# Performance work log

Measured on AMD Instinct MI355X. Metric: run time of the kernel, lower is better.

## Reference

```python
import jax, jax.numpy as jnp
import numpy as np

D = 2048          # hidden_size
E = 32            # num_experts
DFF = 1024        # moe_intermediate_size
T = 1024          # tokens (batch*seq)
TOP_K = 4         # num_experts_per_token
N_GROUP = 4
TOPK_GROUP = 2
SCALING = 2.5     # routed_scaling_factor
N_SHARED = 1
SHARED_DFF = DFF * N_SHARED


def setup_inputs() -> dict:
    key = jax.random.key(0)
    ks = jax.random.split(key, 9)
    def init(k, shape, fan_in):
        return jax.random.normal(k, shape, jnp.float32) * (fan_in ** -0.5)
    return {
        "x": jax.random.normal(ks[0], (T, D), jnp.float32),
        "gate_w": init(ks[1], (E, D), D),                 # router Linear weight [out,in]
        "bias": jnp.zeros((E,), jnp.float32),             # e_score_correction_bias
        "Wg": init(ks[2], (E, DFF, D), D),                # expert gate_proj
        "Wu": init(ks[3], (E, DFF, D), D),                # expert up_proj
        "Wd": init(ks[4], (E, D, DFF), DFF),              # expert down_proj
        "sWg": init(ks[5], (SHARED_DFF, D), D),           # shared expert
        "sWu": init(ks[6], (SHARED_DFF, D), D),
        "sWd": init(ks[7], (D, SHARED_DFF), SHARED_DFF),
    }


def _group_expert_select(gates, bias):
    # gates: [T, E]
    scores = jax.nn.sigmoid(gates)            # score_function='sigmoid'
    orig = scores
    scores = scores + bias
    Eg = E // N_GROUP
    s = scores.reshape(-1, N_GROUP, Eg)       # [T, G, Eg]
    group_scores = jax.lax.top_k(s, 2)[0].sum(-1)          # [T, G] sum of top-2 per group
    k = N_GROUP - TOPK_GROUP
    gidx = jax.lax.top_k(group_scores, k)[1]               # [T, k] largest-scoring groups
    # faithful to torch scatter_ with index shape [...,k,1]: only column 0 of
    # the selected groups is marked True; everything else is zeroed.
    mask = jnp.zeros(s.shape, bool)
    t_idx = jnp.arange(s.shape[0])[:, None]
    mask = mask.at[t_idx, gidx, 0].set(True)
    s = jnp.where(mask, s, 0.0)
    scores = s.reshape(-1, E)
    inds = jax.lax.top_k(scores, TOP_K)[1]                 # [T, K]
    w = jnp.take_along_axis(orig, inds, axis=-1)           # gather original scores
    # top_k > 1 and renormalize
    w = w / (w.sum(-1, keepdims=True) + 1e-20)
    return inds, w * SCALING


def _routed_experts(x, inds, w, Wg, Wu, Wd):
    # Combine dispatch + weighted sum: out[t] = sum_k w[t,k] * expert_{inds[t,k]}(x[t]).
    # Equivalently accumulate coeff[t,e] * expert_e(x[t]) with a scan over experts
    # (fixed structural loop over E weight matrices, vectorized over tokens).
    Tn = x.shape[0]
    coeff = jnp.zeros((Tn, E), x.dtype).at[jnp.arange(Tn)[:, None], inds].add(w)  # [T, E]

    def step(acc, we):
        wg, wu, wd, c = we                      # [DFF,D], [DFF,D], [D,DFF], [T]
        h = jax.nn.silu(x @ wg.T) * (x @ wu.T)  # swiglu: [T, DFF]
        return acc + c[:, None] * (h @ wd.T), None

    out, _ = jax.lax.scan(step, jnp.zeros_like(x), (Wg, Wu, Wd, coeff.T))
    return out


def reference(x, gate_w, bias, Wg, Wu, Wd, sWg, sWu, sWd):
    gates = x @ gate_w.T                                   # [T, E]
    inds, w = _group_expert_select(gates, bias)
    out = _routed_experts(x, inds, w, Wg, Wu, Wd)
    shared = (jax.nn.silu(x @ sWg.T) * (x @ sWu.T)) @ sWd.T
    return out + shared
```

## Files before the change

kernel.cpp:

```cpp
#include <hip/hip_runtime.h>
#include <hip/hip_bf16.h>
#include <math.h>

#define DIM  2048
#define NEXP 32
#define DFF  1024
#define NTOK 1024
#define TOPK 4
#define NGRP 4
#define EPG  8
#define SCALE 2.5f

#define BM 128
#define BN 128
#define BK 64
#define MAX_TILES 80
#define MAX_ROWS  10240

typedef unsigned int  uint_t;
typedef unsigned short us_t;

typedef __attribute__((ext_vector_type(8))) short bf16x8;
typedef __attribute__((ext_vector_type(4))) float f32x4;

#define GLOAD_LDS16(g, l) __builtin_amdgcn_global_load_lds( \
    (const __attribute__((address_space(1))) unsigned int*)(g), \
    (__attribute__((address_space(3))) unsigned int*)(l), 16, 0, 0)

__device__ inline us_t f2b(float f) {
  __hip_bfloat16 h = __float2bfloat16(f);
  return *reinterpret_cast<const us_t*>(&h);
}

__device__ inline uint4 cvt8(float4 a, float4 b) {
  uint4 r;
  r.x = (uint_t)f2b(a.x) | ((uint_t)f2b(a.y) << 16);
  r.y = (uint_t)f2b(a.z) | ((uint_t)f2b(a.w) << 16);
  r.z = (uint_t)f2b(b.x) | ((uint_t)f2b(b.y) << 16);
  r.w = (uint_t)f2b(b.z) | ((uint_t)f2b(b.w) << 16);
  return r;
}

__global__ __launch_bounds__(256) void xcast_kernel(const float4* __restrict__ x4,
                                                    uint2* __restrict__ xb4,
                                                    float4* __restrict__ out4) {
  int i = blockIdx.x * 256 + threadIdx.x;
  float4 v = x4[i];
  uint2 o;
  o.x = (uint_t)f2b(v.x) | ((uint_t)f2b(v.y) << 16);
  o.y = (uint_t)f2b(v.z) | ((uint_t)f2b(v.w) << 16);
  xb4[i] = o;
  out4[i] = make_float4(0.f, 0.f, 0.f, 0.f);
}

__global__ __launch_bounds__(64) void router_kernel(const float* __restrict__ x,
                                                    const float* __restrict__ gw,
                                                    const float* __restrict__ bias,
                                                    int* __restrict__ inds,
                                                    float* __restrict__ wts) {
  int t = blockIdx.x, l = threadIdx.x;
  float xr[32];
#pragma unroll
  for (int i = 0; i < 32; i++) xr[i] = x[t * DIM + i * 64 + l];
  __shared__ float lg[NEXP];
  for (int e = 0; e < NEXP; e++) {
    const float* w = gw + e * DIM;
    float acc = 0.f;
#pragma unroll
    for (int i = 0; i < 32; i++) acc += xr[i] * w[i * 64 + l];
#pragma unroll
    for (int off = 32; off > 0; off >>= 1) acc += __shfl_xor(acc, off);
    if (l == 0) lg[e] = acc;
  }
  __syncthreads();
  if (l != 0) return;

  float s[NEXP], sb[NEXP], mv[NEXP];
#pragma unroll
  for (int e = 0; e < NEXP; e++) {
    float sv = 1.f / (1.f + expf(-lg[e]));
    s[e] = sv; sb[e] = sv + bias[e];
  }
  float gs[NGRP];
#pragma unroll
  for (int g = 0; g < NGRP; g++) {
    float m1 = -1e30f, m2 = -1e30f;
#pragma unroll
    for (int j = 0; j < EPG; j++) {
      float v = sb[g * EPG + j];
      if (v > m1) { m2 = m1; m1 = v; } else if (v > m2) { m2 = v; }
    }
    gs[g] = m1 + m2;
  }
  int g1 = 0;
#pragma unroll
  for (int g = 1; g < NGRP; g++) if (gs[g] > gs[g1]) g1 = g;
  int g2 = -1; float g2v = -1e30f;
#pragma unroll
  for (int g = 0; g < NGRP; g++) {
    if (g == g1) continue;
    if (gs[g] > g2v) { g2v = gs[g]; g2 = g; }
  }
#pragma unroll
  for (int e = 0; e < NEXP; e++) {
    bool keep = (e == g1 * EPG) || (e == g2 * EPG);
    mv[e] = keep ? sb[e] : 0.f;
  }
  uint_t used = 0; float wsum = 0.f;
  int id[TOPK]; float wv[TOPK];
#pragma unroll
  for (int kk = 0; kk < TOPK; kk++) {
    float bv = -1e30f, bs = 0.f; int best = 0;
#pragma unroll
    for (int e = 0; e < NEXP; e++) {
      bool ok = !((used >> e) & 1u) && (mv[e] > bv);
      if (ok) { bv = mv[e]; best = e; bs = s[e]; }
    }
    used |= (1u << best);
    id[kk] = best; wv[kk] = bs; wsum += bs;
  }
  float inv = SCALE / (wsum + 1e-20f);
#pragma unroll
  for (int kk = 0; kk < TOPK; kk++) {
    inds[t * TOPK + kk] = id[kk];
    wts[t * TOPK + kk] = wv[kk] * inv;
  }
}

__global__ __launch_bounds__(256) void plan_kernel(const int* __restrict__ inds,
                                                   const float* __restrict__ wts,
                                                   int* __restrict__ row2tok,
                                                   float* __restrict__ roww,
                                                   int* __restrict__ tileE,
                                                   int* __restrict__ tileR,
                                                   int* __restrict__ nT) {
  __shared__ int wsum[4];
  __shared__ int s_off, s_nt;
  int tid = threadIdx.x, lane = tid & 63, wv = tid >> 6;
  if (tid == 0) { s_off = 0; s_nt = 0; }
  int tb = tid * 4;
  int myi[16];
#pragma unroll
  for (int j = 0; j < 4; j++)
#pragma unroll
    for (int k = 0; k < TOPK; k++) myi[j * 4 + k] = inds[(tb + j) * TOPK + k];
  __syncthreads();
  for (int e = 0; e < NEXP; e++) {
    int off0 = s_off;
    int slot[4]; int cnt = 0;
#pragma unroll
    for (int j = 0; j < 4; j++) {
      int sl = -1;
#pragma unroll
      for (int k = 0; k < TOPK; k++) if (myi[j * 4 + k] == e) sl = k;
      slot[j] = sl; cnt += (sl >= 0) ? 1 : 0;
    }
    int v = cnt;
#pragma unroll
    for (int off = 1; off < 64; off <<= 1) {
      int u = __shfl_up(v, (unsigned)off);
      if (lane >= off) v += u;
    }
    if (lane == 63) wsum[wv] = v;
    __syncthreads();
    int base = 0;
#pragma unroll
    for (int w = 0; w < 4; w++) base += (w < wv) ? wsum[w] : 0;
    int total = wsum[0] + wsum[1] + wsum[2] + wsum[3];
    int r = off0 + base + v - cnt;
#pragma unroll
    for (int j = 0; j < 4; j++) {
      if (slot[j] >= 0) {
        int t = tb + j;
        row2tok[r] = t; roww[r] = wts[t * TOPK + slot[j]];
        r++;
      }
    }
    int ntm = (total + BM - 1) / BM;
    int padEnd = off0 + ntm * BM;
    for (int q = off0 + total + tid; q < padEnd; q += 256) { row2tok[q] = 0; roww[q] = 0.f; }
    __syncthreads();
    if (tid == 0) {
      for (int i = 0; i < ntm; i++) { tileE[s_nt + i] = e; tileR[s_nt + i] = off0 + i * BM; }
      s_nt += ntm; s_off = padEnd;
    }
    __syncthreads();
  }
  int off0 = s_off;
  for (int t = tid; t < NTOK; t += 256) { row2tok[off0 + t] = t; roww[off0 + t] = 1.f; }
  if (tid == 0) {
    for (int i = 0; i < NTOK / BM; i++) { tileE[s_nt + i] = NEXP; tileR[s_nt + i] = off0 + i * BM; }
    nT[0] = s_nt + NTOK / BM;
  }
}

__global__ __launch_bounds__(512) void gateup_kernel(const us_t* __restrict__ xb,
                                                     const float* __restrict__ Wg,
                                                     const float* __restrict__ Wu,
                                                     const float* __restrict__ sWg,
                                                     const float* __restrict__ sWu,
                                                     const int* __restrict__ row2tok,
                                                     const int* __restrict__ tileE,
                                                     const int* __restrict__ tileR,
                                                     const int* __restrict__ nT,
                                                     us_t* __restrict__ H) {
  int hw = blockIdx.x;
  int work = (hw & 7) * (MAX_TILES * (DFF / BN) / 8) + (hw >> 3);
  int tile = work % MAX_TILES;
  int n0 = (work / MAX_TILES) * BN;
  if (tile >= nT[0]) return;
  int e = tileE[tile], row0 = tileR[tile];
  const float* wgp = (e < NEXP) ? (Wg + (size_t)e * DFF * DIM) : sWg;
  const float* wup = (e < NEXP) ? (Wu + (size_t)e * DFF * DIM) : sWu;

  __shared__ us_t Xs[BM][BK];
  __shared__ us_t Gs[BN][BK];
  __shared__ us_t Us[BN][BK];

  int tid = threadIdx.x;
  int lane = tid & 63;
  int wid = tid >> 6;
  int wmr = (wid >> 2) * 64;
  int wnc = (wid & 3) * 32;

  int s0 = wid * 128 + lane, s1 = s0 + 64;
  int xr0 = s0 >> 3, xc0 = s0 & 7;
  int xr1 = s1 >> 3, xc1 = s1 & 7;
  const us_t* xsrc0 = xb + (size_t)row2tok[row0 + xr0] * DIM + (xc0 ^ (xr0 & 7)) * 8;
  const us_t* xsrc1 = xb + (size_t)row2tok[row0 + xr1] * DIM + (xc1 ^ (xr1 & 7)) * 8;
  us_t* xdst0 = &Xs[0][0] + (size_t)(wid * 128) * 8;
  us_t* xdst1 = xdst0 + 64 * 8;

  int a0 = tid, a1 = tid + 512;
  int ar0 = a0 >> 3, ac0 = a0 & 7;
  int ar1 = a1 >> 3, ac1 = a1 & 7;
  const float* gsrc0 = wgp + (size_t)(n0 + ar0) * DIM + (ac0 ^ (ar0 & 7)) * 8;
  const float* gsrc1 = wgp + (size_t)(n0 + ar1) * DIM + (ac1 ^ (ar1 & 7)) * 8;
  const float* usrc0 = wup + (size_t)(n0 + ar0) * DIM + (ac0 ^ (ar0 & 7)) * 8;
  const float* usrc1 = wup + (size_t)(n0 + ar1) * DIM + (ac1 ^ (ar1 & 7)) * 8;
  uint4* gdst0 = (uint4*)((char*)&Gs[0][0] + (size_t)a0 * 16);
  uint4* gdst1 = (uint4*)((char*)&Gs[0][0] + (size_t)a1 * 16);
  uint4* udst0 = (uint4*)((char*)&Us[0][0] + (size_t)a0 * 16);
  uint4* udst1 = (uint4*)((char*)&Us[0][0] + (size_t)a1 * 16);

  f32x4 accg[4][2] = {};
  f32x4 accu[4][2] = {};

  for (int kt = 0; kt < DIM; kt += BK) {
    GLOAD_LDS16(xsrc0 + kt, xdst0);
    GLOAD_LDS16(xsrc1 + kt, xdst1);
    {
      const float4* p = (const float4*)(gsrc0 + kt); *gdst0 = cvt8(p[0], p[1]);
      p = (const float4*)(gsrc1 + kt);               *gdst1 = cvt8(p[0], p[1]);
      p = (const float4*)(usrc0 + kt);               *udst0 = cvt8(p[0], p[1]);
      p = (const float4*)(usrc1 + kt);               *udst1 = cvt8(p[0], p[1]);
    }
    __syncthreads();
#pragma unroll
    for (int ks = 0; ks < BK; ks += 32) {
      int cb = (ks >> 3) + (lane >> 4);
      bf16x8 af[4], bg[2], bu[2];
#pragma unroll
      for (int mi = 0; mi < 4; mi++) {
        int r = wmr + mi * 16 + (lane & 15);
        af[mi] = *(const bf16x8*)&(((const uint4*)&Xs[r][0])[cb ^ (r & 7)]);
      }
#pragma unroll
      for (int ni = 0; ni < 2; ni++) {
        int r = wnc + ni * 16 + (lane & 15);
        bg[ni] = *(const bf16x8*)&(((const uint4*)&Gs[r][0])[cb ^ (r & 7)]);
        bu[ni] = *(const bf16x8*)&(((const uint4*)&Us[r][0])[cb ^ (r & 7)]);
      }
#pragma unroll
      for (int mi = 0; mi < 4; mi++)
#pragma unroll
        for (int ni = 0; ni < 2; ni++) {
          accg[mi][ni] = __builtin_amdgcn_mfma_f32_16x16x32_bf16(af[mi], bg[ni], accg[mi][ni], 0, 0, 0);
          accu[mi][ni] = __builtin_amdgcn_mfma_f32_16x16x32_bf16(af[mi], bu[ni], accu[mi][ni], 0, 0, 0);
        }
    }
    __syncthreads();
  }
#pragma unroll
  for (int mi = 0; mi < 4; mi++) {
#pragma unroll
    for (int j = 0; j < 4; j++) {
      int r = row0 + wmr + mi * 16 + (lane >> 4) * 4 + j;
      us_t* hrow = H + (size_t)r * DFF;
#pragma unroll
      for (int ni = 0; ni < 2; ni++) {
        float g = accg[mi][ni][j], u = accu[mi][ni][j];
        float h = (g / (1.f + expf(-g))) * u;
        hrow[n0 + wnc + ni * 16 + (lane & 15)] = f2b(h);
      }
    }
  }
}

__global__ __launch_bounds__(512) void down_kernel(const us_t* __restrict__ H,
                                                   const float* __restrict__ Wd,
                                                   const float* __restrict__ sWd,
                                                   const int* __restrict__ row2tok,
                                                   const float* __restrict__ roww,
                                                   const int* __restrict__ tileE,
                                                   const int* __restrict__ tileR,
                                                   const int* __restrict__ nT,
                                                   float* __restrict__ out) {
  int hw = blockIdx.x;
  int work = (hw & 7) * (MAX_TILES * (DIM / BN) / 8) + (hw >> 3);
  int tile = work % MAX_TILES;
  int n0 = (work / MAX_TILES) * BN;
  if (tile >= nT[0]) return;
  int e = tileE[tile], row0 = tileR[tile];
  const float* wd = (e < NEXP) ? (Wd + (size_t)e * DIM * DFF) : sWd;

  __shared__ us_t Hs[BM][BK];
  __shared__ us_t Ds[BN][BK];

  int tid = threadIdx.x;
  int lane = tid & 63;
  int wid = tid >> 6;
  int wmr = (wid >> 2) * 64;
  int wnc = (wid & 3) * 32;

  int s0 = wid * 128 + lane, s1 = s0 + 64;
  int hr0 = s0 >> 3, hc0 = s0 & 7;
  int hr1 = s1 >> 3, hc1 = s1 & 7;
  const us_t* hsrc0 = H + (size_t)(row0 + hr0) * DFF + (hc0 ^ (hr0 & 7)) * 8;
  const us_t* hsrc1 = H + (size_t)(row0 + hr1) * DFF + (hc1 ^ (hr1 & 7)) * 8;
  us_t* hdst0 = &Hs[0][0] + (size_t)(wid * 128) * 8;
  us_t* hdst1 = hdst0 + 64 * 8;

  int a0 = tid, a1 = tid + 512;
  int ar0 = a0 >> 3, ac0 = a0 & 7;
  int ar1 = a1 >> 3, ac1 = a1 & 7;
  const float* dsrc0 = wd + (size_t)(n0 + ar0) * DFF + (ac0 ^ (ar0 & 7)) * 8;
  const float* dsrc1 = wd + (size_t)(n0 + ar1) * DFF + (ac1 ^ (ar1 & 7)) * 8;
  uint4* ddst0 = (uint4*)((char*)&Ds[0][0] + (size_t)a0 * 16);
  uint4* ddst1 = (uint4*)((char*)&Ds[0][0] + (size_t)a1 * 16);

  f32x4 acc[4][2] = {};

  for (int kt = 0; kt < DFF; kt += BK) {
    GLOAD_LDS16(hsrc0 + kt, hdst0);
    GLOAD_LDS16(hsrc1 + kt, hdst1);
    {
      const float4* p = (const float4*)(dsrc0 + kt); *ddst0 = cvt8(p[0], p[1]);
      p = (const float4*)(dsrc1 + kt);               *ddst1 = cvt8(p[0], p[1]);
    }
    __syncthreads();
#pragma unroll
    for (int ks = 0; ks < BK; ks += 32) {
      int cb = (ks >> 3) + (lane >> 4);
      bf16x8 af[4], bw[2];
#pragma unroll
      for (int mi = 0; mi < 4; mi++) {
        int r = wmr + mi * 16 + (lane & 15);
        af[mi] = *(const bf16x8*)&(((const uint4*)&Hs[r][0])[cb ^ (r & 7)]);
      }
#pragma unroll
      for (int ni = 0; ni < 2; ni++) {
        int r = wnc + ni * 16 + (lane & 15);
        bw[ni] = *(const bf16x8*)&(((const uint4*)&Ds[r][0])[cb ^ (r & 7)]);
      }
#pragma unroll
      for (int mi = 0; mi < 4; mi++)
#pragma unroll
        for (int ni = 0; ni < 2; ni++)
          acc[mi][ni] = __builtin_amdgcn_mfma_f32_16x16x32_bf16(af[mi], bw[ni], acc[mi][ni], 0, 0, 0);
    }
    __syncthreads();
  }
#pragma unroll
  for (int mi = 0; mi < 4; mi++) {
#pragma unroll
    for (int j = 0; j < 4; j++) {
      int r = row0 + wmr + mi * 16 + (lane >> 4) * 4 + j;
      float wgt = roww[r];
      int tok = row2tok[r];
      float* orow = out + (size_t)tok * DIM;
#pragma unroll
      for (int ni = 0; ni < 2; ni++)
        atomicAdd(orow + n0 + wnc + ni * 16 + (lane & 15), acc[mi][ni][j] * wgt);
    }
  }
}

extern "C" void kernel_launch(void* const* d_in, const int* in_sizes, int n_in,
                              void* d_out, int out_size, void* d_ws, size_t ws_size,
                              hipStream_t stream) {
  const float* x    = (const float*)d_in[0];
  const float* gw   = (const float*)d_in[1];
  const float* bias = (const float*)d_in[2];
  const float* Wg   = (const float*)d_in[3];
  const float* Wu   = (const float*)d_in[4];
  const float* Wd   = (const float*)d_in[5];
  const float* sWg  = (const float*)d_in[6];
  const float* sWu  = (const float*)d_in[7];
  const float* sWd  = (const float*)d_in[8];
  float* out = (float*)d_out;

  char* p = (char*)d_ws;
  us_t* xb = (us_t*)p;            p += (size_t)NTOK * DIM * 2;
  us_t* H  = (us_t*)p;            p += (size_t)MAX_ROWS * DFF * 2;
  int* inds = (int*)p;            p += NTOK * TOPK * 4;
  float* wts = (float*)p;         p += NTOK * TOPK * 4;
  int* row2tok = (int*)p;         p += MAX_ROWS * 4;
  float* roww = (float*)p;        p += MAX_ROWS * 4;
  int* tileE = (int*)p;           p += MAX_TILES * 4;
  int* tileR = (int*)p;           p += MAX_TILES * 4;
  int* nT = (int*)p;              p += 4;

  hipLaunchKernelGGL(xcast_kernel, dim3(NTOK * DIM / 1024), dim3(256), 0, stream,
                     (const float4*)x, (uint2*)xb, (float4*)out);
  hipLaunchKernelGGL(router_kernel, dim3(NTOK), dim3(64), 0, stream, x, gw, bias, inds, wts);
  hipLaunchKernelGGL(plan_kernel, dim3(1), dim3(256), 0, stream,
                     inds, wts, row2tok, roww, tileE, tileR, nT);
  hipLaunchKernelGGL(gateup_kernel, dim3(MAX_TILES * (DFF / BN)), dim3(512), 0, stream,
                     xb, Wg, Wu, sWg, sWu, row2tok, tileE, tileR, nT, H);
  hipLaunchKernelGGL(down_kernel, dim3(MAX_TILES * (DIM / BN)), dim3(512), 0, stream,
                     H, Wd, sWd, row2tok, roww, tileE, tileR, nT, out);
}
```

Baseline: 244.1 us.

## Double-buffer LDS in gate/up and down GEMMs; two tokens per router block

Gives the gate/up and down GEMM kernels double-buffered shared-memory tiles. The next K-slice's global loads (X/H via direct-to-LDS, fp32 weights into registers) are issued before computing on the current buffer, and the converted weights are written to the other buffer afterwards. The aim is to hide global load latency behind MFMA work, at the cost of doubled LDS usage and more live registers, which may lower occupancy. The router kernel now handles two tokens per block so each gate-weight load is reused across both tokens.

```diff
diff --git a/kernel.cpp b/kernel.cpp
--- a/kernel.cpp
+++ b/kernel.cpp
@@ -58,27 +58,37 @@
                                                     const float* __restrict__ bias,
                                                     int* __restrict__ inds,
                                                     float* __restrict__ wts) {
-  int t = blockIdx.x, l = threadIdx.x;
-  float xr[32];
-#pragma unroll
-  for (int i = 0; i < 32; i++) xr[i] = x[t * DIM + i * 64 + l];
-  __shared__ float lg[NEXP];
+  int t0 = blockIdx.x * 2, l = threadIdx.x;
+  float xa[32], xc[32];
+#pragma unroll
+  for (int i = 0; i < 32; i++) {
+    xa[i] = x[(size_t)t0 * DIM + i * 64 + l];
+    xc[i] = x[(size_t)(t0 + 1) * DIM + i * 64 + l];
+  }
+  __shared__ float lg[2][NEXP];
   for (int e = 0; e < NEXP; e++) {
     const float* w = gw + e * DIM;
-    float acc = 0.f;
-#pragma unroll
-    for (int i = 0; i < 32; i++) acc += xr[i] * w[i * 64 + l];
-#pragma unroll
-    for (int off = 32; off > 0; off >>= 1) acc += __shfl_xor(acc, off);
-    if (l == 0) lg[e] = acc;
+    float a0 = 0.f, a1 = 0.f;
+#pragma unroll
+    for (int i = 0; i < 32; i++) {
+      float wv = w[i * 64 + l];
+      a0 += xa[i] * wv; a1 += xc[i] * wv;
+    }
+#pragma unroll
+    for (int off = 32; off > 0; off >>= 1) {
+      a0 += __shfl_xor(a0, off);
+      a1 += __shfl_xor(a1, off);
+    }
+    if (l == 0) { lg[0][e] = a0; lg[1][e] = a1; }
   }
   __syncthreads();
-  if (l != 0) return;
+  if (l >= 2) return;
+  int t = t0 + l;
 
   float s[NEXP], sb[NEXP], mv[NEXP];
 #pragma unroll
   for (int e = 0; e < NEXP; e++) {
-    float sv = 1.f / (1.f + expf(-lg[e]));
+    float sv = 1.f / (1.f + expf(-lg[l][e]));
     s[e] = sv; sb[e] = sv + bias[e];
   }
   float gs[NGRP];
@@ -213,9 +223,9 @@
   const float* wgp = (e < NEXP) ? (Wg + (size_t)e * DFF * DIM) : sWg;
   const float* wup = (e < NEXP) ? (Wu + (size_t)e * DFF * DIM) : sWu;
 
-  __shared__ us_t Xs[BM][BK];
-  __shared__ us_t Gs[BN][BK];
-  __shared__ us_t Us[BN][BK];
+  __shared__ us_t Xs[2][BM][BK];
+  __shared__ us_t Gs[2][BN][BK];
+  __shared__ us_t Us[2][BN][BK];
 
   int tid = threadIdx.x;
   int lane = tid & 63;
@@ -228,8 +238,8 @@
   int xr1 = s1 >> 3, xc1 = s1 & 7;
   const us_t* xsrc0 = xb + (size_t)row2tok[row0 + xr0] * DIM + (xc0 ^ (xr0 & 7)) * 8;
   const us_t* xsrc1 = xb + (size_t)row2tok[row0 + xr1] * DIM + (xc1 ^ (xr1 & 7)) * 8;
-  us_t* xdst0 = &Xs[0][0] + (size_t)(wid * 128) * 8;
-  us_t* xdst1 = xdst0 + 64 * 8;
+  size_t xdo0 = (size_t)(wid * 128) * 8;
+  size_t xdo1 = xdo0 + 64 * 8;
 
   int a0 = tid, a1 = tid + 512;
   int ar0 = a0 >> 3, ac0 = a0 & 7;
@@ -238,49 +248,75 @@
   const float* gsrc1 = wgp + (size_t)(n0 + ar1) * DIM + (ac1 ^ (ar1 & 7)) * 8;
   const float* usrc0 = wup + (size_t)(n0 + ar0) * DIM + (ac0 ^ (ar0 & 7)) * 8;
   const float* usrc1 = wup + (size_t)(n0 + ar1) * DIM + (ac1 ^ (ar1 & 7)) * 8;
-  uint4* gdst0 = (uint4*)((char*)&Gs[0][0] + (size_t)a0 * 16);
-  uint4* gdst1 = (uint4*)((char*)&Gs[0][0] + (size_t)a1 * 16);
-  uint4* udst0 = (uint4*)((char*)&Us[0][0] + (size_t)a0 * 16);
-  uint4* udst1 = (uint4*)((char*)&Us[0][0] + (size_t)a1 * 16);
 
   f32x4 accg[4][2] = {};
   f32x4 accu[4][2] = {};
 
-  for (int kt = 0; kt < DIM; kt += BK) {
-    GLOAD_LDS16(xsrc0 + kt, xdst0);
-    GLOAD_LDS16(xsrc1 + kt, xdst1);
-    {
-      const float4* p = (const float4*)(gsrc0 + kt); *gdst0 = cvt8(p[0], p[1]);
-      p = (const float4*)(gsrc1 + kt);               *gdst1 = cvt8(p[0], p[1]);
-      p = (const float4*)(usrc0 + kt);               *udst0 = cvt8(p[0], p[1]);
-      p = (const float4*)(usrc1 + kt);               *udst1 = cvt8(p[0], p[1]);
-    }
-    __syncthreads();
-#pragma unroll
-    for (int ks = 0; ks < BK; ks += 32) {
-      int cb = (ks >> 3) + (lane >> 4);
-      bf16x8 af[4], bg[2], bu[2];
-#pragma unroll
-      for (int mi = 0; mi < 4; mi++) {
-        int r = wmr + mi * 16 + (lane & 15);
-        af[mi] = *(const bf16x8*)&(((const uint4*)&Xs[r][0])[cb ^ (r & 7)]);
-      }
-#pragma unroll
-      for (int ni = 0; ni < 2; ni++) {
-        int r = wnc + ni * 16 + (lane & 15);
-        bg[ni] = *(const bf16x8*)&(((const uint4*)&Gs[r][0])[cb ^ (r & 7)]);
-        bu[ni] = *(const bf16x8*)&(((const uint4*)&Us[r][0])[cb ^ (r & 7)]);
-      }
-#pragma unroll
-      for (int mi = 0; mi < 4; mi++)
-#pragma unroll
-        for (int ni = 0; ni < 2; ni++) {
-          accg[mi][ni] = __builtin_amdgcn_mfma_f32_16x16x32_bf16(af[mi], bg[ni], accg[mi][ni], 0, 0, 0);
-          accu[mi][ni] = __builtin_amdgcn_mfma_f32_16x16x32_bf16(af[mi], bu[ni], accu[mi][ni], 0, 0, 0);
-        }
-    }
-    __syncthreads();
-  }
+#define GU_ISSUE_X(B, KT) do { \
+    GLOAD_LDS16(xsrc0 + (KT), &Xs[B][0][0] + xdo0); \
+    GLOAD_LDS16(xsrc1 + (KT), &Xs[B][0][0] + xdo1); } while (0)
+
+#define GU_LOAD_W(KT, G0, G1, G2, G3, U0, U1, U2, U3) do { \
+    const float4* p_; \
+    p_ = (const float4*)(gsrc0 + (KT)); G0 = p_[0]; G1 = p_[1]; \
+    p_ = (const float4*)(gsrc1 + (KT)); G2 = p_[0]; G3 = p_[1]; \
+    p_ = (const float4*)(usrc0 + (KT)); U0 = p_[0]; U1 = p_[1]; \
+    p_ = (const float4*)(usrc1 + (KT)); U2 = p_[0]; U3 = p_[1]; } while (0)
+
+#define GU_WRITE_W(B, G0, G1, G2, G3, U0, U1, U2, U3) do { \
+    ((uint4*)((char*)&Gs[B][0][0] + (size_t)a0 * 16))[0] = cvt8(G0, G1); \
+    ((uint4*)((char*)&Gs[B][0][0] + (size_t)a1 * 16))[0] = cvt8(G2, G3); \
+    ((uint4*)((char*)&Us[B][0][0] + (size_t)a0 * 16))[0] = cvt8(U0, U1); \
+    ((uint4*)((char*)&Us[B][0][0] + (size_t)a1 * 16))[0] = cvt8(U2, U3); } while (0)
+
+#define GU_COMPUTE(B) do { \
+    _Pragma("unroll") \
+    for (int ks = 0; ks < BK; ks += 32) { \
+      int cb = (ks >> 3) + (lane >> 4); \
+      bf16x8 af[4], bg[2], bu[2]; \
+      _Pragma("unroll") \
+      for (int mi = 0; mi < 4; mi++) { \
+        int r = wmr + mi * 16 + (lane & 15); \
+        af[mi] = *(const bf16x8*)&(((const uint4*)&Xs[B][r][0])[cb ^ (r & 7)]); \
+      } \
+      _Pragma("unroll") \
+      for (int ni = 0; ni < 2; ni++) { \
+        int r = wnc + ni * 16 + (lane & 15); \
+        bg[ni] = *(const bf16x8*)&(((const uint4*)&Gs[B][r][0])[cb ^ (r & 7)]); \
+        bu[ni] = *(const bf16x8*)&(((const uint4*)&Us[B][r][0])[cb ^ (r & 7)]); \
+      } \
+      _Pragma("unroll") \
+      for (int mi = 0; mi < 4; mi++) \
+        _Pragma("unroll") \
+        for (int ni = 0; ni < 2; ni++) { \
+          accg[mi][ni] = __builtin_amdgcn_mfma_f32_16x16x32_bf16(af[mi], bg[ni], accg[mi][ni], 0, 0, 0); \
+          accu[mi][ni] = __builtin_amdgcn_mfma_f32_16x16x32_bf16(af[mi], bu[ni], accu[mi][ni], 0, 0, 0); \
+        } \
+    } } while (0)
+
+  float4 g0, g1, g2, g3, u0, u1, u2, u3;
+  GU_ISSUE_X(0, 0);
+  GU_LOAD_W(0, g0, g1, g2, g3, u0, u1, u2, u3);
+  GU_WRITE_W(0, g0, g1, g2, g3, u0, u1, u2, u3);
+  __syncthreads();
+
+  for (int kt = 0; kt < DIM; kt += 2 * BK) {
+    int ktB = kt + BK, ktN = kt + 2 * BK;
+    bool more = (ktN < DIM);
+    GU_ISSUE_X(1, ktB);
+    GU_LOAD_W(ktB, g0, g1, g2, g3, u0, u1, u2, u3);
+    GU_COMPUTE(0);
+    GU_WRITE_W(1, g0, g1, g2, g3, u0, u1, u2, u3);
+    __syncthreads();
+    if (more) {
+      GU_ISSUE_X(0, ktN);
+      GU_LOAD_W(ktN, g0, g1, g2, g3, u0, u1, u2, u3);
+    }
+    GU_COMPUTE(1);
+    if (more) GU_WRITE_W(0, g0, g1, g2, g3, u0, u1, u2, u3);
+    __syncthreads();
+  }
+
 #pragma unroll
   for (int mi = 0; mi < 4; mi++) {
 #pragma unroll
@@ -314,8 +350,8 @@
   int e = tileE[tile], row0 = tileR[tile];
   const float* wd = (e < NEXP) ? (Wd + (size_t)e * DIM * DFF) : sWd;
 
-  __shared__ us_t Hs[BM][BK];
-  __shared__ us_t Ds[BN][BK];
+  __shared__ us_t Hs[2][BM][BK];
+  __shared__ us_t Ds[2][BN][BK];
 
   int tid = threadIdx.x;
   int lane = tid & 63;
@@ -328,49 +364,75 @@
   int hr1 = s1 >> 3, hc1 = s1 & 7;
   const us_t* hsrc0 = H + (size_t)(row0 + hr0) * DFF + (hc0 ^ (hr0 & 7)) * 8;
   const us_t* hsrc1 = H + (size_t)(row0 + hr1) * DFF + (hc1 ^ (hr1 & 7)) * 8;
-  us_t* hdst0 = &Hs[0][0] + (size_t)(wid * 128) * 8;
-  us_t* hdst1 = hdst0 + 64 * 8;
+  size_t hdo0 = (size_t)(wid * 128) * 8;
+  size_t hdo1 = hdo0 + 64 * 8;
 
   int a0 = tid, a1 = tid + 512;
   int ar0 = a0 >> 3, ac0 = a0 & 7;
   int ar1 = a1 >> 3, ac1 = a1 & 7;
   const float* dsrc0 = wd + (size_t)(n0 + ar0) * DFF + (ac0 ^ (ar0 & 7)) * 8;
   const float* dsrc1 = wd + (size_t)(n0 + ar1) * DFF + (ac1 ^ (ar1 & 7)) * 8;
-  uint4* ddst0 = (uint4*)((char*)&Ds[0][0] + (size_t)a0 * 16);
-  uint4* ddst1 = (uint4*)((char*)&Ds[0][0] + (size_t)a1 * 16);
 
   f32x4 acc[4][2] = {};
 
-  for (int kt = 0; kt < DFF; kt += BK) {
-    GLOAD_LDS16(hsrc0 + kt, hdst0);
-    GLOAD_LDS16(hsrc1 + kt, hdst1);
-    {
-      const float4* p = (const float4*)(dsrc0 + kt); *ddst0 = cvt8(p[0], p[1]);
-      p = (const float4*)(dsrc1 + kt);               *ddst1 = cvt8(p[0], p[1]);
-    }
-    __syncthreads();
-#pragma unroll
-    for (int ks = 0; ks < BK; ks += 32) {
-      int cb = (ks >> 3) + (lane >> 4);
-      bf16x8 af[4], bw[2];
-#pragma unroll
-      for (int mi = 0; mi < 4; mi++) {
-        int r = wmr + mi * 16 + (lane & 15);
-        af[mi] = *(const bf16x8*)&(((const uint4*)&Hs[r][0])[cb ^ (r & 7)]);
-      }
-#pragma unroll
-      for (int ni = 0; ni < 2; ni++) {
-        int r = wnc + ni * 16 + (lane & 15);
-        bw[ni] = *(const bf16x8*)&(((const uint4*)&Ds[r][0])[cb ^ (r & 7)]);
-      }
-#pragma unroll
-      for (int mi = 0; mi < 4; mi++)
-#pragma unroll
-        for (int ni = 0; ni < 2; ni++)
-          acc[mi][ni] = __builtin_amdgcn_mfma_f32_16x16x32_bf16(af[mi], bw[ni], acc[mi][ni], 0, 0, 0);
-    }
-    __syncthreads();
-  }
+#define DN_ISSUE_H(B, KT) do { \
+    GLOAD_LDS16(hsrc0 + (KT), &Hs[B][0][0] + hdo0); \
+    GLOAD_LDS16(hsrc1 + (KT), &Hs[B][0][0] + hdo1); } while (0)
+
+#define DN_LOAD_W(KT, D0, D1, D2, D3) do { \
+    const float4* p_; \
+    p_ = (const float4*)(dsrc0 + (KT)); D0 = p_[0]; D1 = p_[1]; \
+    p_ = (const float4*)(dsrc1 + (KT)); D2 = p_[0]; D3 = p_[1]; } while (0)
+
+#define DN_WRITE_W(B, D0, D1, D2, D3) do { \
+    ((uint4*)((char*)&Ds[B][0][0] + (size_t)a0 * 16))[0] = cvt8(D0, D1); \
+    ((uint4*)((char*)&Ds[B][0][0] + (size_t)a1 * 16))[0] = cvt8(D2, D3); } while (0)
+
+#define DN_COMPUTE(B) do { \
+    _Pragma("unroll") \
+    for (int ks = 0; ks < BK; ks += 32) { \
+      int cb = (ks >> 3) + (lane >> 4); \
+      bf16x8 af[4], bw[2]; \
+      _Pragma("unroll") \
+      for (int mi = 0; mi < 4; mi++) { \
+        int r = wmr + mi * 16 + (lane & 15); \
+        af[mi] = *(const bf16x8*)&(((const uint4*)&Hs[B][r][0])[cb ^ (r & 7)]); \
+      } \
+      _Pragma("unroll") \
+      for (int ni = 0; ni < 2; ni++) { \
+        int r = wnc + ni * 16 + (lane & 15); \
+        bw[ni] = *(const bf16x8*)&(((const uint4*)&Ds[B][r][0])[cb ^ (r & 7)]); \
+      } \
+      _Pragma("unroll") \
+      for (int mi = 0; mi < 4; mi++) \
+        _Pragma("unroll") \
+        for (int ni = 0; ni < 2; ni++) \
+          acc[mi][ni] = __builtin_amdgcn_mfma_f32_16x16x32_bf16(af[mi], bw[ni], acc[mi][ni], 0, 0, 0); \
+    } } while (0)
+
+  float4 d0, d1, d2, d3;
+  DN_ISSUE_H(0, 0);
+  DN_LOAD_W(0, d0, d1, d2, d3);
+  DN_WRITE_W(0, d0, d1, d2, d3);
+  __syncthreads();
+
+  for (int kt = 0; kt < DFF; kt += 2 * BK) {
+    int ktB = kt + BK, ktN = kt + 2 * BK;
+    bool more = (ktN < DFF);
+    DN_ISSUE_H(1, ktB);
+    DN_LOAD_W(ktB, d0, d1, d2, d3);
+    DN_COMPUTE(0);
+    DN_WRITE_W(1, d0, d1, d2, d3);
+    __syncthreads();
+    if (more) {
+      DN_ISSUE_H(0, ktN);
+      DN_LOAD_W(ktN, d0, d1, d2, d3);
+    }
+    DN_COMPUTE(1);
+    if (more) DN_WRITE_W(0, d0, d1, d2, d3);
+    __syncthreads();
+  }
+
 #pragma unroll
   for (int mi = 0; mi < 4; mi++) {
 #pragma unroll
@@ -413,7 +475,7 @@
 
   hipLaunchKernelGGL(xcast_kernel, dim3(NTOK * DIM / 1024), dim3(256), 0, stream,
                      (const float4*)x, (uint2*)xb, (float4*)out);
-  hipLaunchKernelGGL(router_kernel, dim3(NTOK), dim3(64), 0, stream, x, gw, bias, inds, wts);
+  hipLaunchKernelGGL(router_kernel, dim3(NTOK / 2), dim3(64), 0, stream, x, gw, bias, inds, wts);
   hipLaunchKernelGGL(plan_kernel, dim3(1), dim3(256), 0, stream,
                      inds, wts, row2tok, roww, tileE, tileR, nT);
   hipLaunchKernelGGL(gateup_kernel, dim3(MAX_TILES * (DFF / BN)), dim3(512), 0, stream,
```

Measured after the change: 281.7 us. 15.4% more time.

## Pre-convert active expert weights to bf16 once and load them via LDS DMA

Applied to the files above, without the earlier changes.

The plan kernel now records up to 8 active experts into compact slots. A new wconv kernel converts only those experts' gate, up and down weights, plus the shared expert's, to bf16 in a workspace. The GEMM kernels then stream bf16 weights straight into LDS with global_load_lds, instead of reading fp32 and converting in registers on every tile. The router also handles two tokens per block so each gate-weight load is shared. The cost is an extra conversion pass and a large workspace, and any expert beyond the 8-slot cap is silently dropped, which leans on the sparse routing this reference produces.

```diff
diff --git a/kernel.cpp b/kernel.cpp
--- a/kernel.cpp
+++ b/kernel.cpp
@@ -16,6 +16,8 @@
 #define BK 64
 #define MAX_TILES 80
 #define MAX_ROWS  10240
+#define MAXACT 8
+#define SLOT_ELEMS (2048 * 1024)
 
 typedef unsigned int  uint_t;
 typedef unsigned short us_t;
@@ -30,15 +32,6 @@
 __device__ inline us_t f2b(float f) {
   __hip_bfloat16 h = __float2bfloat16(f);
   return *reinterpret_cast<const us_t*>(&h);
-}
-
-__device__ inline uint4 cvt8(float4 a, float4 b) {
-  uint4 r;
-  r.x = (uint_t)f2b(a.x) | ((uint_t)f2b(a.y) << 16);
-  r.y = (uint_t)f2b(a.z) | ((uint_t)f2b(a.w) << 16);
-  r.z = (uint_t)f2b(b.x) | ((uint_t)f2b(b.y) << 16);
-  r.w = (uint_t)f2b(b.z) | ((uint_t)f2b(b.w) << 16);
-  return r;
 }
 
 __global__ __launch_bounds__(256) void xcast_kernel(const float4* __restrict__ x4,
@@ -58,27 +51,37 @@
                                                     const float* __restrict__ bias,
                                                     int* __restrict__ inds,
                                                     float* __restrict__ wts) {
-  int t = blockIdx.x, l = threadIdx.x;
-  float xr[32];
-#pragma unroll
-  for (int i = 0; i < 32; i++) xr[i] = x[t * DIM + i * 64 + l];
-  __shared__ float lg[NEXP];
+  int t0 = blockIdx.x * 2, l = threadIdx.x;
+  float xa[32], xc[32];
+#pragma unroll
+  for (int i = 0; i < 32; i++) {
+    xa[i] = x[(size_t)t0 * DIM + i * 64 + l];
+    xc[i] = x[(size_t)(t0 + 1) * DIM + i * 64 + l];
+  }
+  __shared__ float lg[2][NEXP];
   for (int e = 0; e < NEXP; e++) {
     const float* w = gw + e * DIM;
-    float acc = 0.f;
-#pragma unroll
-    for (int i = 0; i < 32; i++) acc += xr[i] * w[i * 64 + l];
-#pragma unroll
-    for (int off = 32; off > 0; off >>= 1) acc += __shfl_xor(acc, off);
-    if (l == 0) lg[e] = acc;
+    float a0 = 0.f, a1 = 0.f;
+#pragma unroll
+    for (int i = 0; i < 32; i++) {
+      float wv = w[i * 64 + l];
+      a0 += xa[i] * wv; a1 += xc[i] * wv;
+    }
+#pragma unroll
+    for (int off = 32; off > 0; off >>= 1) {
+      a0 += __shfl_xor(a0, off);
+      a1 += __shfl_xor(a1, off);
+    }
+    if (l == 0) { lg[0][e] = a0; lg[1][e] = a1; }
   }
   __syncthreads();
-  if (l != 0) return;
+  if (l >= 2) return;
+  int t = t0 + l;
 
   float s[NEXP], sb[NEXP], mv[NEXP];
 #pragma unroll
   for (int e = 0; e < NEXP; e++) {
-    float sv = 1.f / (1.f + expf(-lg[e]));
+    float sv = 1.f / (1.f + expf(-lg[l][e]));
     s[e] = sv; sb[e] = sv + bias[e];
   }
   float gs[NGRP];
@@ -131,13 +134,15 @@
                                                    const float* __restrict__ wts,
                                                    int* __restrict__ row2tok,
                                                    float* __restrict__ roww,
-                                                   int* __restrict__ tileE,
+                                                   int* __restrict__ tileS,
                                                    int* __restrict__ tileR,
-                                                   int* __restrict__ nT) {
+                                                   int* __restrict__ nT,
+                                                   int* __restrict__ actE,
+                                                   int* __restrict__ nAct) {
   __shared__ int wsum[4];
-  __shared__ int s_off, s_nt;
+  __shared__ int s_off, s_nt, s_na;
   int tid = threadIdx.x, lane = tid & 63, wv = tid >> 6;
-  if (tid == 0) { s_off = 0; s_nt = 0; }
+  if (tid == 0) { s_off = 0; s_nt = 0; s_na = 0; }
   int tb = tid * 4;
   int myi[16];
 #pragma unroll
@@ -180,8 +185,10 @@
     int padEnd = off0 + ntm * BM;
     for (int q = off0 + total + tid; q < padEnd; q += 256) { row2tok[q] = 0; roww[q] = 0.f; }
     __syncthreads();
-    if (tid == 0) {
-      for (int i = 0; i < ntm; i++) { tileE[s_nt + i] = e; tileR[s_nt + i] = off0 + i * BM; }
+    if (tid == 0 && ntm > 0 && s_na < MAXACT) {
+      int sl = s_na;
+      actE[sl] = e; s_na = sl + 1;
+      for (int i = 0; i < ntm; i++) { tileS[s_nt + i] = sl; tileR[s_nt + i] = off0 + i * BM; }
       s_nt += ntm; s_off = padEnd;
     }
     __syncthreads();
@@ -189,18 +196,62 @@
   int off0 = s_off;
   for (int t = tid; t < NTOK; t += 256) { row2tok[off0 + t] = t; roww[off0 + t] = 1.f; }
   if (tid == 0) {
-    for (int i = 0; i < NTOK / BM; i++) { tileE[s_nt + i] = NEXP; tileR[s_nt + i] = off0 + i * BM; }
+    for (int i = 0; i < NTOK / BM; i++) { tileS[s_nt + i] = s_na; tileR[s_nt + i] = off0 + i * BM; }
     nT[0] = s_nt + NTOK / BM;
+    nAct[0] = s_na;
+  }
+}
+
+__global__ __launch_bounds__(256) void wconv_kernel(const float* __restrict__ Wg,
+                                                    const float* __restrict__ Wu,
+                                                    const float* __restrict__ Wd,
+                                                    const float* __restrict__ sWg,
+                                                    const float* __restrict__ sWu,
+                                                    const float* __restrict__ sWd,
+                                                    const int* __restrict__ actE,
+                                                    const int* __restrict__ nAct,
+                                                    us_t* __restrict__ Wgb,
+                                                    us_t* __restrict__ Wub,
+                                                    us_t* __restrict__ Wdb) {
+  int slot = blockIdx.y;
+  int na = nAct[0];
+  const float *sg, *su, *sd;
+  size_t dslot;
+  if (slot < MAXACT) {
+    if (slot >= na) return;
+    int e = actE[slot];
+    sg = Wg + (size_t)e * SLOT_ELEMS;
+    su = Wu + (size_t)e * SLOT_ELEMS;
+    sd = Wd + (size_t)e * SLOT_ELEMS;
+    dslot = (size_t)slot;
+  } else {
+    sg = sWg; su = sWu; sd = sWd;
+    dslot = (size_t)na;
+  }
+  size_t tbase = (size_t)blockIdx.x * 256 + threadIdx.x;
+  const float* srcs[3] = { sg, su, sd };
+  us_t* dsts[3] = { Wgb + dslot * SLOT_ELEMS, Wub + dslot * SLOT_ELEMS, Wdb + dslot * SLOT_ELEMS };
+#pragma unroll
+  for (int m = 0; m < 3; m++) {
+    const float4* s4 = (const float4*)srcs[m];
+    uint2* d2 = (uint2*)dsts[m];
+#pragma unroll
+    for (int i = 0; i < 4; i++) {
+      size_t idx = tbase + (size_t)i * 131072;
+      float4 v = s4[idx];
+      uint2 o;
+      o.x = (uint_t)f2b(v.x) | ((uint_t)f2b(v.y) << 16);
+      o.y = (uint_t)f2b(v.z) | ((uint_t)f2b(v.w) << 16);
+      d2[idx] = o;
+    }
   }
 }
 
 __global__ __launch_bounds__(512) void gateup_kernel(const us_t* __restrict__ xb,
-                                                     const float* __restrict__ Wg,
-                                                     const float* __restrict__ Wu,
-                                                     const float* __restrict__ sWg,
-                                                     const float* __restrict__ sWu,
+                                                     const us_t* __restrict__ Wgb,
+                                                     const us_t* __restrict__ Wub,
                                                      const int* __restrict__ row2tok,
-                                                     const int* __restrict__ tileE,
+                                                     const int* __restrict__ tileS,
                                                      const int* __restrict__ tileR,
                                                      const int* __restrict__ nT,
                                                      us_t* __restrict__ H) {
@@ -209,9 +260,9 @@
   int tile = work % MAX_TILES;
   int n0 = (work / MAX_TILES) * BN;
   if (tile >= nT[0]) return;
-  int e = tileE[tile], row0 = tileR[tile];
-  const float* wgp = (e < NEXP) ? (Wg + (size_t)e * DFF * DIM) : sWg;
-  const float* wup = (e < NEXP) ? (Wu + (size_t)e * DFF * DIM) : sWu;
+  int sl = tileS[tile], row0 = tileR[tile];
+  const us_t* wgp = Wgb + (size_t)sl * SLOT_ELEMS;
+  const us_t* wup = Wub + (size_t)sl * SLOT_ELEMS;
 
   __shared__ us_t Xs[BM][BK];
   __shared__ us_t Gs[BN][BK];
@@ -224,37 +275,27 @@
   int wnc = (wid & 3) * 32;
 
   int s0 = wid * 128 + lane, s1 = s0 + 64;
-  int xr0 = s0 >> 3, xc0 = s0 & 7;
-  int xr1 = s1 >> 3, xc1 = s1 & 7;
-  const us_t* xsrc0 = xb + (size_t)row2tok[row0 + xr0] * DIM + (xc0 ^ (xr0 & 7)) * 8;
-  const us_t* xsrc1 = xb + (size_t)row2tok[row0 + xr1] * DIM + (xc1 ^ (xr1 & 7)) * 8;
-  us_t* xdst0 = &Xs[0][0] + (size_t)(wid * 128) * 8;
-  us_t* xdst1 = xdst0 + 64 * 8;
-
-  int a0 = tid, a1 = tid + 512;
-  int ar0 = a0 >> 3, ac0 = a0 & 7;
-  int ar1 = a1 >> 3, ac1 = a1 & 7;
-  const float* gsrc0 = wgp + (size_t)(n0 + ar0) * DIM + (ac0 ^ (ar0 & 7)) * 8;
-  const float* gsrc1 = wgp + (size_t)(n0 + ar1) * DIM + (ac1 ^ (ar1 & 7)) * 8;
-  const float* usrc0 = wup + (size_t)(n0 + ar0) * DIM + (ac0 ^ (ar0 & 7)) * 8;
-  const float* usrc1 = wup + (size_t)(n0 + ar1) * DIM + (ac1 ^ (ar1 & 7)) * 8;
-  uint4* gdst0 = (uint4*)((char*)&Gs[0][0] + (size_t)a0 * 16);
-  uint4* gdst1 = (uint4*)((char*)&Gs[0][0] + (size_t)a1 * 16);
-  uint4* udst0 = (uint4*)((char*)&Us[0][0] + (size_t)a0 * 16);
-  uint4* udst1 = (uint4*)((char*)&Us[0][0] + (size_t)a1 * 16);
+  int r0 = s0 >> 3, c0 = s0 & 7;
+  int r1 = s1 >> 3, c1 = s1 & 7;
+  const us_t* xsrc0 = xb + (size_t)row2tok[row0 + r0] * DIM + (c0 ^ (r0 & 7)) * 8;
+  const us_t* xsrc1 = xb + (size_t)row2tok[row0 + r1] * DIM + (c1 ^ (r1 & 7)) * 8;
+  const us_t* gsrc0 = wgp + (size_t)(n0 + r0) * DIM + (c0 ^ (r0 & 7)) * 8;
+  const us_t* gsrc1 = wgp + (size_t)(n0 + r1) * DIM + (c1 ^ (r1 & 7)) * 8;
+  const us_t* usrc0 = wup + (size_t)(n0 + r0) * DIM + (c0 ^ (r0 & 7)) * 8;
+  const us_t* usrc1 = wup + (size_t)(n0 + r1) * DIM + (c1 ^ (r1 & 7)) * 8;
+  size_t do0 = (size_t)(wid * 128) * 8;
+  size_t do1 = do0 + 64 * 8;
 
   f32x4 accg[4][2] = {};
   f32x4 accu[4][2] = {};
 
   for (int kt = 0; kt < DIM; kt += BK) {
-    GLOAD_LDS16(xsrc0 + kt, xdst0);
-    GLOAD_LDS16(xsrc1 + kt, xdst1);
-    {
-      const float4* p = (const float4*)(gsrc0 + kt); *gdst0 = cvt8(p[0], p[1]);
-      p = (const float4*)(gsrc1 + kt);               *gdst1 = cvt8(p[0], p[1]);
-      p = (const float4*)(usrc0 + kt);               *udst0 = cvt8(p[0], p[1]);
-      p = (const float4*)(usrc1 + kt);               *udst1 = cvt8(p[0], p[1]);
-    }
+    GLOAD_LDS16(xsrc0 + kt, &Xs[0][0] + do0);
+    GLOAD_LDS16(xsrc1 + kt, &Xs[0][0] + do1);
+    GLOAD_LDS16(gsrc0 + kt, &Gs[0][0] + do0);
+    GLOAD_LDS16(gsrc1 + kt, &Gs[0][0] + do1);
+    GLOAD_LDS16(usrc0 + kt, &Us[0][0] + do0);
+    GLOAD_LDS16(usrc1 + kt, &Us[0][0] + do1);
     __syncthreads();
 #pragma unroll
     for (int ks = 0; ks < BK; ks += 32) {
@@ -298,11 +339,10 @@
 }
 
 __global__ __launch_bounds__(512) void down_kernel(const us_t* __restrict__ H,
-                                                   const float* __restrict__ Wd,
-                                                   const float* __restrict__ sWd,
+                                                   const us_t* __restrict__ Wdb,
                                                    const int* __restrict__ row2tok,
                                                    const float* __restrict__ roww,
-                                                   const int* __restrict__ tileE,
+                                                   const int* __restrict__ tileS,
                                                    const int* __restrict__ tileR,
                                                    const int* __restrict__ nT,
                                                    float* __restrict__ out) {
@@ -311,8 +351,8 @@
   int tile = work % MAX_TILES;
   int n0 = (work / MAX_TILES) * BN;
   if (tile >= nT[0]) return;
-  int e = tileE[tile], row0 = tileR[tile];
-  const float* wd = (e < NEXP) ? (Wd + (size_t)e * DIM * DFF) : sWd;
+  int sl = tileS[tile], row0 = tileR[tile];
+  const us_t* wd = Wdb + (size_t)sl * SLOT_ELEMS;
 
   __shared__ us_t Hs[BM][BK];
   __shared__ us_t Ds[BN][BK];
@@ -324,30 +364,22 @@
   int wnc = (wid & 3) * 32;
 
   int s0 = wid * 128 + lane, s1 = s0 + 64;
-  int hr0 = s0 >> 3, hc0 = s0 & 7;
-  int hr1 = s1 >> 3, hc1 = s1 & 7;
-  const us_t* hsrc0 = H + (size_t)(row0 + hr0) * DFF + (hc0 ^ (hr0 & 7)) * 8;
-  const us_t* hsrc1 = H + (size_t)(row0 + hr1) * DFF + (hc1 ^ (hr1 & 7)) * 8;
-  us_t* hdst0 = &Hs[0][0] + (size_t)(wid * 128) * 8;
-  us_t* hdst1 = hdst0 + 64 * 8;
-
-  int a0 = tid, a1 = tid + 512;
-  int ar0 = a0 >> 3, ac0 = a0 & 7;
-  int ar1 = a1 >> 3, ac1 = a1 & 7;
-  const float* dsrc0 = wd + (size_t)(n0 + ar0) * DFF + (ac0 ^ (ar0 & 7)) * 8;
-  const float* dsrc1 = wd + (size_t)(n0 + ar1) * DFF + (ac1 ^ (ar1 & 7)) * 8;
-  uint4* ddst0 = (uint4*)((char*)&Ds[0][0] + (size_t)a0 * 16);
-  uint4* ddst1 = (uint4*)((char*)&Ds[0][0] + (size_t)a1 * 16);
+  int r0 = s0 >> 3, c0 = s0 & 7;
+  int r1 = s1 >> 3, c1 = s1 & 7;
+  const us_t* hsrc0 = H + (size_t)(row0 + r0) * DFF + (c0 ^ (r0 & 7)) * 8;
+  const us_t* hsrc1 = H + (size_t)(row0 + r1) * DFF + (c1 ^ (r1 & 7)) * 8;
+  const us_t* dsrc0 = wd + (size_t)(n0 + r0) * DFF + (c0 ^ (r0 & 7)) * 8;
+  const us_t* dsrc1 = wd + (size_t)(n0 + r1) * DFF + (c1 ^ (r1 & 7)) * 8;
+  size_t do0 = (size_t)(wid * 128) * 8;
+  size_t do1 = do0 + 64 * 8;
 
   f32x4 acc[4][2] = {};
 
   for (int kt = 0; kt < DFF; kt += BK) {
-    GLOAD_LDS16(hsrc0 + kt, hdst0);
-    GLOAD_LDS16(hsrc1 + kt, hdst1);
-    {
-      const float4* p = (const float4*)(dsrc0 + kt); *ddst0 = cvt8(p[0], p[1]);
-      p = (const float4*)(dsrc1 + kt);               *ddst1 = cvt8(p[0], p[1]);
-    }
+    GLOAD_LDS16(hsrc0 + kt, &Hs[0][0] + do0);
+    GLOAD_LDS16(hsrc1 + kt, &Hs[0][0] + do1);
+    GLOAD_LDS16(dsrc0 + kt, &Ds[0][0] + do0);
+    GLOAD_LDS16(dsrc1 + kt, &Ds[0][0] + do1);
     __syncthreads();
 #pragma unroll
     for (int ks = 0; ks < BK; ks += 32) {
@@ -401,23 +433,30 @@
   float* out = (float*)d_out;
 
   char* p = (char*)d_ws;
-  us_t* xb = (us_t*)p;            p += (size_t)NTOK * DIM * 2;
-  us_t* H  = (us_t*)p;            p += (size_t)MAX_ROWS * DFF * 2;
+  us_t* xb  = (us_t*)p;           p += (size_t)NTOK * DIM * 2;
+  us_t* H   = (us_t*)p;           p += (size_t)MAX_ROWS * DFF * 2;
+  us_t* Wgb = (us_t*)p;           p += (size_t)(MAXACT + 1) * SLOT_ELEMS * 2;
+  us_t* Wub = (us_t*)p;           p += (size_t)(MAXACT + 1) * SLOT_ELEMS * 2;
+  us_t* Wdb = (us_t*)p;           p += (size_t)(MAXACT + 1) * SLOT_ELEMS * 2;
   int* inds = (int*)p;            p += NTOK * TOPK * 4;
   float* wts = (float*)p;         p += NTOK * TOPK * 4;
   int* row2tok = (int*)p;         p += MAX_ROWS * 4;
   float* roww = (float*)p;        p += MAX_ROWS * 4;
-  int* tileE = (int*)p;           p += MAX_TILES * 4;
+  int* tileS = (int*)p;           p += MAX_TILES * 4;
   int* tileR = (int*)p;           p += MAX_TILES * 4;
   int* nT = (int*)p;              p += 4;
+  int* actE = (int*)p;            p += MAXACT * 4;
+  int* nAct = (int*)p;            p += 4;
 
   hipLaunchKernelGGL(xcast_kernel, dim3(NTOK * DIM / 1024), dim3(256), 0, stream,
                      (const float4*)x, (uint2*)xb, (float4*)out);
-  hipLaunchKernelGGL(router_kernel, dim3(NTOK), dim3(64), 0, stream, x, gw, bias, inds, wts);
+  hipLaunchKernelGGL(router_kernel, dim3(NTOK / 2), dim3(64), 0, stream, x, gw, bias, inds, wts);
   hipLaunchKernelGGL(plan_kernel, dim3(1), dim3(256), 0, stream,
-                     inds, wts, row2tok, roww, tileE, tileR, nT);
+                     inds, wts, row2tok, roww, tileS, tileR, nT, actE, nAct);
+  hipLaunchKernelGGL(wconv_kernel, dim3(512, MAXACT + 1), dim3(256), 0, stream,
+                     Wg, Wu, Wd, sWg, sWu, sWd, actE, nAct, Wgb, Wub, Wdb);
   hipLaunchKernelGGL(gateup_kernel, dim3(MAX_TILES * (DFF / BN)), dim3(512), 0, stream,
-                     xb, Wg, Wu, sWg, sWu, row2tok, tileE, tileR, nT, H);
+                     xb, Wgb, Wub, row2tok, tileS, tileR, nT, H);
   hipLaunchKernelGGL(down_kernel, dim3(MAX_TILES * (DIM / BN)), dim3(512), 0, stream,
-                     H, Wd, sWd, row2tok, roww, tileE, tileR, nT, out);
-}
+                     H, Wdb, row2tok, roww, tileS, tileR, nT, out);
+}
```

Result: no change. 245.1 us (+0.4%).
